# Optimization experiments

Measured on AMD Instinct MI355X. Metric: run time of the kernel, lower is better.

The kernel has to match this reference:

```python
import jax, jax.numpy as jnp
import numpy as np

EPSILON = 1e-06


def setup_inputs() -> dict:
    key = jax.random.key(0)
    k1, k2 = jax.random.split(key)
    logits = jax.random.normal(k1, (16, 2, 1024, 1024), dtype=jnp.float32)
    labels = jax.random.randint(k2, (16, 1, 1024, 1024), 0, 2, dtype=jnp.int32)
    return {"logits": logits, "labels": labels}


def reference(logits, labels):
    # Build one-hot targets: channel 0 = background (label==0), channel 1 = foreground.
    t = labels.astype(bool)                      # [B,1,H,W]
    targets = jnp.concatenate([jnp.logical_not(t), t], axis=1).astype(jnp.float32)  # [B,2,H,W]
    probs = jax.nn.softmax(logits, axis=1)       # softmax over class channel
    axes = tuple(range(2, logits.ndim))          # spatial axes (2,3)
    numerator = 2.0 * jnp.sum(targets * probs, axis=axes)               # [B,2]
    denominator = jnp.sum(probs * probs + targets * targets, axis=axes)  # [B,2]
    return 1.0 - jnp.mean(numerator / (denominator + EPSILON))
```

## Files before the change

kernel.cpp:

```cpp
#include <hip/hip_runtime.h>

constexpr int HW = 1024 * 1024;
constexpr int NB = 16;
constexpr float EPS = 1e-6f;
constexpr int BLOCKS_PER_BATCH = 128;
constexpr int THREADS = 256;
constexpr int NVEC    = HW / 4;
constexpr int TPB     = BLOCKS_PER_BATCH * THREADS;
constexpr int U       = NVEC / TPB;
constexpr int NBLK    = NB * BLOCKS_PER_BATCH;

typedef float f32x4 __attribute__((ext_vector_type(4)));
typedef int   i32x4 __attribute__((ext_vector_type(4)));

__global__ __launch_bounds__(THREADS, 8) void dice_partial(
        const float* __restrict__ logits,
        const int*   __restrict__ labels,
        f32x4*       __restrict__ ws4) {
    const int b   = blockIdx.x >> 7;
    const int blk = blockIdx.x & 127;

    const f32x4* __restrict__ L0 = reinterpret_cast<const f32x4*>(logits + (size_t)b * 2 * HW);
    const f32x4* __restrict__ L1 = reinterpret_cast<const f32x4*>(logits + (size_t)b * 2 * HW + HW);
    const i32x4* __restrict__ LB = reinterpret_cast<const i32x4*>(labels + (size_t)b * HW);

    const int base = blk * THREADS + threadIdx.x;

    float sp = 0.f, spp = 0.f, st = 0.f, stp = 0.f;

    #pragma unroll
    for (int u = 0; u < U; ++u) {
        const int i = base + u * TPB;
        f32x4 a = __builtin_nontemporal_load(&L0[i]);
        f32x4 c = __builtin_nontemporal_load(&L1[i]);
        i32x4 t = __builtin_nontemporal_load(&LB[i]);

        #pragma unroll
        for (int k = 0; k < 4; ++k) {
            const float p  = 1.f / (1.f + __expf(a[k] - c[k]));
            const float tf = (float)t[k];
            sp += p; spp = fmaf(p, p, spp); st += tf; stp = fmaf(tf, p, stp);
        }
    }

    #pragma unroll
    for (int off = 32; off > 0; off >>= 1) {
        sp  += __shfl_down(sp,  off);
        spp += __shfl_down(spp, off);
        st  += __shfl_down(st,  off);
        stp += __shfl_down(stp, off);
    }

    __shared__ float red[4][4];
    const int wave = threadIdx.x >> 6;
    const int lane = threadIdx.x & 63;
    if (lane == 0) {
        red[wave][0] = sp; red[wave][1] = spp; red[wave][2] = st; red[wave][3] = stp;
    }
    __syncthreads();
    if (threadIdx.x == 0) {
        f32x4 r;
        r.x = red[0][0] + red[1][0] + red[2][0] + red[3][0];
        r.y = red[0][1] + red[1][1] + red[2][1] + red[3][1];
        r.z = red[0][2] + red[1][2] + red[2][2] + red[3][2];
        r.w = red[0][3] + red[1][3] + red[2][3] + red[3][3];
        ws4[blockIdx.x] = r;
    }
}

__global__ __launch_bounds__(128) void dice_batch(
        const f32x4* __restrict__ ws4,
        float*       __restrict__ terms) {
    const int b = blockIdx.x;
    f32x4 v = ws4[b * BLOCKS_PER_BATCH + threadIdx.x];

    #pragma unroll
    for (int off = 32; off > 0; off >>= 1) {
        v.x += __shfl_down(v.x, off);
        v.y += __shfl_down(v.y, off);
        v.z += __shfl_down(v.z, off);
        v.w += __shfl_down(v.w, off);
    }

    __shared__ f32x4 red[2];
    const int wave = threadIdx.x >> 6;
    const int lane = threadIdx.x & 63;
    if (lane == 0) red[wave] = v;
    __syncthreads();
    if (threadIdx.x == 0) {
        const float Sp  = red[0].x + red[1].x;
        const float Spp = red[0].y + red[1].y;
        const float St  = red[0].z + red[1].z;
        const float Stp = red[0].w + red[1].w;
        const float N = (float)HW;

        const float num1 = 2.f * Stp;
        const float den1 = Spp + St;
        const float num0 = 2.f * (N - St - Sp + Stp);
        const float den0 = (N - 2.f * Sp + Spp) + (N - St);

        terms[b] = num0 / (den0 + EPS) + num1 / (den1 + EPS);
    }
}

__global__ void dice_final(const float* __restrict__ terms, float* __restrict__ out) {
    float local = (threadIdx.x < NB) ? terms[threadIdx.x] : 0.f;
    #pragma unroll
    for (int off = 32; off > 0; off >>= 1) local += __shfl_down(local, off);
    if (threadIdx.x == 0) out[0] = 1.f - local / 32.f;
}

extern "C" void kernel_launch(void* const* d_in, const int* in_sizes, int n_in,
                              void* d_out, int out_size, void* d_ws, size_t ws_size,
                              hipStream_t stream) {
    const float* logits = (const float*)d_in[0];
    const int*   labels = (const int*)d_in[1];
    float* out   = (float*)d_out;
    f32x4* ws4   = (f32x4*)d_ws;
    float* terms = (float*)d_ws + NBLK * 4;

    dice_partial<<<NBLK, THREADS, 0, stream>>>(logits, labels, ws4);
    dice_batch<<<NB, 128, 0, stream>>>(ws4, terms);
    dice_final<<<1, 64, 0, stream>>>(terms, out);
}
```

Baseline: 221.1 us.

## Software-pipeline partial loads and merge batch/final reductions into one kernel

Adds an explicit two-deep register prefetch in the streaming loop so the loads for iteration u+2 are issued before computing iteration u. It also fuses the per-batch reduction and the final scalar reduction into a single 1024-thread kernel, one wave per batch, which removes one kernel launch. The loop is fully unrolled, so the compiler may already have hoisted these loads, and holding the extra buffers raises register pressure.

```diff
diff --git a/kernel.cpp b/kernel.cpp
--- a/kernel.cpp
+++ b/kernel.cpp
@@ -26,21 +26,36 @@
 
     const int base = blk * THREADS + threadIdx.x;
 
+    f32x4 a[2], c[2];
+    i32x4 t[2];
+    a[0] = __builtin_nontemporal_load(&L0[base]);
+    c[0] = __builtin_nontemporal_load(&L1[base]);
+    t[0] = __builtin_nontemporal_load(&LB[base]);
+    a[1] = __builtin_nontemporal_load(&L0[base + TPB]);
+    c[1] = __builtin_nontemporal_load(&L1[base + TPB]);
+    t[1] = __builtin_nontemporal_load(&LB[base + TPB]);
+
     float sp = 0.f, spp = 0.f, st = 0.f, stp = 0.f;
 
     #pragma unroll
     for (int u = 0; u < U; ++u) {
-        const int i = base + u * TPB;
-        f32x4 a = __builtin_nontemporal_load(&L0[i]);
-        f32x4 c = __builtin_nontemporal_load(&L1[i]);
-        i32x4 t = __builtin_nontemporal_load(&LB[i]);
-
+        const int cur = u & 1;
+        f32x4 an, cn;
+        i32x4 tn;
+        const bool pf = (u + 2 < U);
+        if (pf) {
+            const int i = base + (u + 2) * TPB;
+            an = __builtin_nontemporal_load(&L0[i]);
+            cn = __builtin_nontemporal_load(&L1[i]);
+            tn = __builtin_nontemporal_load(&LB[i]);
+        }
         #pragma unroll
         for (int k = 0; k < 4; ++k) {
-            const float p  = 1.f / (1.f + __expf(a[k] - c[k]));
-            const float tf = (float)t[k];
+            const float p  = 1.f / (1.f + __expf(a[cur][k] - c[cur][k]));
+            const float tf = (float)t[cur][k];
             sp += p; spp = fmaf(p, p, spp); st += tf; stp = fmaf(tf, p, stp);
         }
+        if (pf) { a[cur] = an; c[cur] = cn; t[cur] = tn; }
     }
 
     #pragma unroll
@@ -68,11 +83,14 @@
     }
 }
 
-__global__ __launch_bounds__(128) void dice_batch(
+__global__ __launch_bounds__(1024) void dice_reduce(
         const f32x4* __restrict__ ws4,
-        float*       __restrict__ terms) {
-    const int b = blockIdx.x;
-    f32x4 v = ws4[b * BLOCKS_PER_BATCH + threadIdx.x];
+        float*       __restrict__ out) {
+    const int wave = threadIdx.x >> 6;
+    const int lane = threadIdx.x & 63;
+
+    f32x4 v = ws4[wave * BLOCKS_PER_BATCH + lane]
+            + ws4[wave * BLOCKS_PER_BATCH + 64 + lane];
 
     #pragma unroll
     for (int off = 32; off > 0; off >>= 1) {
@@ -82,16 +100,12 @@
         v.w += __shfl_down(v.w, off);
     }
 
-    __shared__ f32x4 red[2];
-    const int wave = threadIdx.x >> 6;
-    const int lane = threadIdx.x & 63;
-    if (lane == 0) red[wave] = v;
-    __syncthreads();
-    if (threadIdx.x == 0) {
-        const float Sp  = red[0].x + red[1].x;
-        const float Spp = red[0].y + red[1].y;
-        const float St  = red[0].z + red[1].z;
-        const float Stp = red[0].w + red[1].w;
+    __shared__ float terms[NB];
+    if (lane == 0) {
+        const float Sp  = v.x;
+        const float Spp = v.y;
+        const float St  = v.z;
+        const float Stp = v.w;
         const float N = (float)HW;
 
         const float num1 = 2.f * Stp;
@@ -99,15 +113,15 @@
         const float num0 = 2.f * (N - St - Sp + Stp);
         const float den0 = (N - 2.f * Sp + Spp) + (N - St);
 
-        terms[b] = num0 / (den0 + EPS) + num1 / (den1 + EPS);
+        terms[wave] = num0 / (den0 + EPS) + num1 / (den1 + EPS);
     }
-}
-
-__global__ void dice_final(const float* __restrict__ terms, float* __restrict__ out) {
-    float local = (threadIdx.x < NB) ? terms[threadIdx.x] : 0.f;
-    #pragma unroll
-    for (int off = 32; off > 0; off >>= 1) local += __shfl_down(local, off);
-    if (threadIdx.x == 0) out[0] = 1.f - local / 32.f;
+    __syncthreads();
+    if (threadIdx.x == 0) {
+        float s = 0.f;
+        #pragma unroll
+        for (int i = 0; i < NB; ++i) s += terms[i];
+        out[0] = 1.f - s / 32.f;
+    }
 }
 
 extern "C" void kernel_launch(void* const* d_in, const int* in_sizes, int n_in,
@@ -115,11 +129,9 @@
                               hipStream_t stream) {
     const float* logits = (const float*)d_in[0];
     const int*   labels = (const int*)d_in[1];
-    float* out   = (float*)d_out;
-    f32x4* ws4   = (f32x4*)d_ws;
-    float* terms = (float*)d_ws + NBLK * 4;
+    float* out = (float*)d_out;
+    f32x4* ws4 = (f32x4*)d_ws;
 
     dice_partial<<<NBLK, THREADS, 0, stream>>>(logits, labels, ws4);
-    dice_batch<<<NB, 128, 0, stream>>>(ws4, terms);
-    dice_final<<<1, 64, 0, stream>>>(terms, out);
+    dice_reduce<<<1, 1024, 0, stream>>>(ws4, out);
 }
```

After: 216.2 us, median of 2. 1.02x faster.
